# Kernel optimization log

Hardware: AMD Instinct MI355X
Metric: run time of the kernel (lower is better)

## Reference

```python
import jax, jax.numpy as jnp
import numpy as np

DIM = 256
NUM_HEADS = 8
NUM_NEI = (16, 32)
G = len(NUM_NEI)          # branches
G_H = NUM_HEADS // G      # heads per branch = 4
G_DIM = DIM // G          # channels per branch = 128
HD = G_DIM // G_H         # head dim = 32
SCALE = HD ** (-0.5)
M_MSF = G                 # MSF branches
CHANNEL = DIM // M_MSF    # 128
D_MSF = CHANNEL           # r=1

gelu = lambda t: jax.nn.gelu(t, approximate=False)


def setup_inputs() -> dict:
    key = jax.random.key(0)
    ks = jax.random.split(key, 16)
    B, N = 4, 2048
    s = lambda fan: fan ** (-0.5)
    inp = {
        "x": jax.random.normal(ks[0], (B, N, DIM), jnp.float32),
        "pos": jax.random.uniform(ks[1], (B, N, 3), jnp.float32),
        # qkv linear (no bias); stored as (in, out)
        "Wqkv": jax.random.normal(ks[2], (DIM, 3 * DIM), jnp.float32) * s(DIM),
        # per-branch rel-pos MLPs: Linear(3, g_dim) + GELU
        "Wp0": jax.random.normal(ks[3], (3, G_DIM), jnp.float32) * s(3),
        "bp0": jnp.zeros((G_DIM,), jnp.float32),
        "Wp1": jax.random.normal(ks[4], (3, G_DIM), jnp.float32) * s(3),
        "bp1": jnp.zeros((G_DIM,), jnp.float32),
        # MSF params
        "W_proj": jax.random.normal(ks[5], (DIM, DIM), jnp.float32) * s(DIM),
        "b_proj": jnp.zeros((DIM,), jnp.float32),
        "W_fc1": jax.random.normal(ks[6], (DIM, D_MSF), jnp.float32) * s(DIM),
        "b_fc1": jnp.zeros((D_MSF,), jnp.float32),
        "W_fc2": jax.random.normal(ks[7], (D_MSF, M_MSF * CHANNEL), jnp.float32) * s(D_MSF),
        "b_fc2": jnp.zeros((M_MSF * CHANNEL,), jnp.float32),
        "W_head": jax.random.normal(ks[8], (DIM, DIM), jnp.float32) * s(DIM),
        "b_head": jnp.zeros((DIM,), jnp.float32),
    }
    return inp


def _branch(q, k, v, pos, knn_idx, Wp, bp):
    """One head-group: KNN gather + rel-pos MLP fused attention.
    q,k,v: [B,N,g_dim]; pos: [B,N,3]; knn_idx: [B,N,nk]."""
    B, N, g_dim = k.shape
    nk = knn_idx.shape[-1]
    gather = jax.vmap(lambda t, idx: t[idx])  # per-batch fancy gather -> [B,N,nk,D]
    knn_xyz = gather(pos, knn_idx)                       # [B,N,nk,3]
    kg = gather(k, knn_idx)                              # [B,N,nk,g_dim]
    vg = gather(v, knn_idx)
    # split heads: b n k (h d) -> b h n k d
    split = lambda t: t.reshape(B, N, nk, G_H, HD).transpose(0, 3, 1, 2, 4)
    kg, vg = split(kg), split(vg)
    rel = pos[:, :, None, :] - knn_xyz                   # [B,N,nk,3]
    vrp = split(gelu(rel @ Wp + bp))                     # [B,h,N,nk,d]
    vg = vg + vrp
    attn_rel = vrp.sum(-1)                               # [B,h,N,nk]
    qh = q.reshape(B, N, G_H, HD).transpose(0, 2, 1, 3)  # [B,h,N,d]
    logits = jnp.einsum('bhnd,bhnkd->bhnk', qh, kg) * SCALE + attn_rel
    a = jax.nn.softmax(logits, axis=-1)
    out = jnp.einsum('bhnk,bhnkd->bhnd', a, vg)          # [B,h,N,d]
    return out.transpose(0, 2, 1, 3).reshape(B, N, g_dim)


def _msf(x, W_proj, b_proj, W_fc1, b_fc1, W_fc2, b_fc2, W_head, b_head):
    bs, N, dim = x.shape
    input_groups = x.transpose(0, 2, 1).reshape(bs, M_MSF, CHANNEL, N)
    feats_proj = gelu(x @ W_proj + b_proj)               # [bs,N,dim]
    feats_S = feats_proj.mean(axis=1)                    # global avg pool over N -> [bs,dim]
    feats_Z = gelu(feats_S @ W_fc1 + b_fc1)
    av = (feats_Z @ W_fc2 + b_fc2).reshape(bs, M_MSF, CHANNEL, 1)
    av = jax.nn.softmax(av, axis=1)                      # softmax over branches
    feats_V = (input_groups * av).reshape(bs, dim, N).transpose(0, 2, 1)
    feats_V = feats_V @ W_head + b_head
    return feats_proj + feats_V


def reference(x, pos, Wqkv, Wp0, bp0, Wp1, bp1,
              W_proj, b_proj, W_fc1, b_fc1, W_fc2, b_fc2, W_head, b_head):
    B, N, C = x.shape
    # pairwise squared distances [B,N,N] (broadcast form, as in source)
    dists = jnp.sum((pos[:, :, None, :] - pos[:, None, :, :]) ** 2, axis=-1)
    order = jnp.argsort(dists, axis=-1)                  # [B,N,N]
    qkv = (x @ Wqkv).reshape(B, N, 3, C).transpose(2, 0, 1, 3)  # [3,B,N,C]
    pos_params = [(Wp0, bp0), (Wp1, bp1)]
    outs = []
    for i, nk in enumerate(NUM_NEI):
        sl = slice(i * G_DIM, (i + 1) * G_DIM)
        q, k, v = qkv[0][..., sl], qkv[1][..., sl], qkv[2][..., sl]
        knn_idx = order[:, :, :nk]
        Wp, bp = pos_params[i]
        outs.append(_branch(q, k, v, pos, knn_idx, Wp, bp))
    xcat = jnp.concatenate(outs, axis=-1)                # [B,N,C]
    return _msf(xcat, W_proj, b_proj, W_fc1, b_fc1, W_fc2, b_fc2, W_head, b_head)
```

## Files before the change

### kernel.cpp

```cpp
#include <hip/hip_runtime.h>
#include <cstdint>
#include <cstddef>

#define B_    4
#define NPT   2048
#define DIM_  256
#define QKVW  768
#define XLEN  2097152
#define QLEN  196608
#define PLEN  65536
#define TOTC  (XLEN + QLEN + 2 * PLEN)

typedef unsigned short ushort_t;
typedef unsigned long long u64;
typedef short bf16x8 __attribute__((ext_vector_type(8)));
typedef float f32x4 __attribute__((ext_vector_type(4)));

__device__ __forceinline__ float gelu_f(float x) {
  return 0.5f * x * (1.0f + erff(x * 0.70710678118654752440f));
}

__device__ __forceinline__ float gelu_fast(float x) {
  const float is2 = 0.70710678118654752440f;
  float z = x * is2;
  float az = __builtin_fabsf(z);
  float t = __builtin_amdgcn_rcpf(fmaf(0.3275911f, az, 1.0f));
  float p = fmaf(1.061405429f, t, -1.453152027f);
  p = fmaf(p, t, 1.421413741f);
  p = fmaf(p, t, -0.284496736f);
  p = fmaf(p, t, 0.254829592f);
  p = p * t;
  float e = __expf(-az * az);
  float er = fmaf(-p, e, 1.0f);
  er = __builtin_copysignf(er, x);
  return 0.5f * x * (1.0f + er);
}

__device__ __forceinline__ ushort_t f2bf(float f) {
  unsigned u = __float_as_uint(f);
  unsigned r = (u + 0x7fffu + ((u >> 16) & 1u)) >> 16;
  return (ushort_t)r;
}
__device__ __forceinline__ float bf2f(ushort_t h) {
  return __uint_as_float(((unsigned)h) << 16);
}
__device__ __forceinline__ float bflo(unsigned p) {
  return __uint_as_float(p << 16);
}
__device__ __forceinline__ float bfhi(unsigned p) {
  return __uint_as_float(p & 0xffff0000u);
}

__device__ __forceinline__ float bfly16_sum(float x) {
  x += __int_as_float(__builtin_amdgcn_ds_swizzle(__float_as_int(x), 0x041F));
  x += __int_as_float(__builtin_amdgcn_ds_swizzle(__float_as_int(x), 0x081F));
  x += __int_as_float(__builtin_amdgcn_ds_swizzle(__float_as_int(x), 0x101F));
  x += __int_as_float(__builtin_amdgcn_ds_swizzle(__float_as_int(x), 0x201F));
  return x;
}

__device__ __forceinline__ bf16x8 scale_bf(bf16x8 v, const float* avk) {
  bf16x8 r;
#pragma unroll
  for (int e = 0; e < 8; e++) {
    float f = bf2f((ushort_t)v[e]) * avk[e];
    r[e] = (short)f2bf(f);
  }
  return r;
}

__global__ __launch_bounds__(256) void convert_kernel(
    const float* __restrict__ x, const float* __restrict__ Wqkv,
    const float* __restrict__ Wproj, const float* __restrict__ Whead,
    ushort_t* __restrict__ xbf, ushort_t* __restrict__ WqkvT,
    ushort_t* __restrict__ WprojT, ushort_t* __restrict__ WheadT,
    float* __restrict__ part) {
  int base = blockIdx.x * 256 + threadIdx.x;
  if (base < 1024) part[base] = 0.f;
  for (int i = base; i < TOTC; i += 2048 * 256) {
    if (i < XLEN) {
      xbf[i] = f2bf(x[i]);
    } else if (i < XLEN + QLEN) {
      int e = i - XLEN;
      int k = e / 768, n = e - k * 768;
      WqkvT[n * 256 + k] = f2bf(Wqkv[e]);
    } else if (i < XLEN + QLEN + PLEN) {
      int e = i - XLEN - QLEN;
      int k = e >> 8, n = e & 255;
      WprojT[n * 256 + k] = f2bf(Wproj[e]);
    } else {
      int e = i - XLEN - QLEN - PLEN;
      int k = e >> 8, n = e & 255;
      WheadT[n * 256 + k] = f2bf(Whead[e]);
    }
  }
}

__global__ __launch_bounds__(256) void knn_gemm0_kernel(
    const float* __restrict__ pos, int* __restrict__ idx_out,
    const ushort_t* __restrict__ A, const ushort_t* __restrict__ BT,
    ushort_t* __restrict__ C) {
  __shared__ u64 buf[3][128];
  int tid = threadIdx.x;
  int w = tid >> 6, lane = tid & 63;
  if (w == 3) {
    constexpr int K = 256;
    constexpr int N = 768;
    int quad = lane >> 4, r16 = lane & 15;
    int t0 = blockIdx.x;
    int m0 = (t0 / 24) * 64, n0 = (t0 % 24) * 32;
    const ushort_t* Ap = A + (size_t)(m0 + r16) * K + quad * 8;
    const ushort_t* Bp = BT + (size_t)(n0 + r16) * K + quad * 8;
    f32x4 acc[4][2] = {};
    bf16x8 af[4], bfv[2], af2[4], bf2[2];
#pragma unroll
    for (int i = 0; i < 4; i++) af[i] = *(const bf16x8*)(Ap + (size_t)i * 16 * K);
#pragma unroll
    for (int j = 0; j < 2; j++) bfv[j] = *(const bf16x8*)(Bp + (size_t)j * 16 * K);
#pragma unroll
    for (int kc = 0; kc < 8; kc++) {
      if (kc < 7) {
        int ko = (kc + 1) * 32;
#pragma unroll
        for (int i = 0; i < 4; i++)
          af2[i] = *(const bf16x8*)(Ap + (size_t)i * 16 * K + ko);
#pragma unroll
        for (int j = 0; j < 2; j++)
          bf2[j] = *(const bf16x8*)(Bp + (size_t)j * 16 * K + ko);
      }
#pragma unroll
      for (int i = 0; i < 4; i++) {
        acc[i][0] = __builtin_amdgcn_mfma_f32_16x16x32_bf16(af[i], bfv[0], acc[i][0], 0, 0, 0);
        acc[i][1] = __builtin_amdgcn_mfma_f32_16x16x32_bf16(af[i], bfv[1], acc[i][1], 0, 0, 0);
      }
#pragma unroll
      for (int i = 0; i < 4; i++) af[i] = af2[i];
      bfv[0] = bf2[0]; bfv[1] = bf2[1];
    }
#pragma unroll
    for (int i = 0; i < 4; i++) {
#pragma unroll
      for (int j = 0; j < 2; j++) {
        int col = n0 + j * 16 + r16;
#pragma unroll
        for (int r = 0; r < 4; r++) {
          int row = m0 + i * 16 + quad * 4 + r;
          C[(size_t)row * N + col] = f2bf(acc[i][j][r]);
        }
      }
    }
    return;
  }
  int wq = blockIdx.x * 3 + w;
  if (wq >= 8192) return;
  int b = wq >> 11, n = wq & (NPT - 1);
  const float* pb = pos + (size_t)b * NPT * 3;
  float qx = pb[n * 3 + 0], qy = pb[n * 3 + 1], qz = pb[n * 3 + 2];
  float dist[32];
  {
#pragma clang fp contract(off)
#pragma unroll
    for (int s = 0; s < 32; s++) {
      int j = lane + (s << 6);
      float dx = qx - pb[j * 3 + 0];
      float dy = qy - pb[j * 3 + 1];
      float dz = qz - pb[j * 3 + 2];
      float d = dx * dx;
      d = d + dy * dy;
      d = d + dz * dz;
      dist[s] = d;
    }
  }
  unsigned lo = 0x3C000000u;
  unsigned hi = 0x3E800001u;
  for (int it = 0; it < 31 && hi - lo > 1; ++it) {
    unsigned mid = (lo + hi) >> 1;
    float fm = __uint_as_float(mid);
    int c = 0;
#pragma unroll
    for (int s = 0; s < 32; s++)
      c += (int)__popcll(__ballot(dist[s] < fm));
    if (c >= 32) { hi = mid; if (c <= 64) break; }
    else lo = mid;
  }
  float fT = __uint_as_float(hi);
  buf[w][lane] = ~0ULL;
  buf[w][lane + 64] = ~0ULL;
  __builtin_amdgcn_wave_barrier();
  asm volatile("s_waitcnt lgkmcnt(0)" ::: "memory");
  unsigned base = 0;
#pragma unroll
  for (int s = 0; s < 32; s++) {
    bool m = dist[s] < fT;
    u64 bal = __ballot(m);
    unsigned pre = __builtin_amdgcn_mbcnt_hi(
        (unsigned)(bal >> 32), __builtin_amdgcn_mbcnt_lo((unsigned)bal, 0u));
    unsigned p = base + pre;
    if (m && p < 128u) {
      int j = lane + (s << 6);
      buf[w][p] = ((u64)__float_as_uint(dist[s]) << 32) | (unsigned)j;
    }
    base += (unsigned)__popcll(bal);
  }
  __builtin_amdgcn_wave_barrier();
  asm volatile("s_waitcnt lgkmcnt(0)" ::: "memory");
  unsigned total = base;
  if (total > 128u) total = 128u;
  unsigned mt = (total + 7u) & ~7u;
  u64 k0 = buf[w][lane];
  u64 k1 = buf[w][lane + 64];
  int r0 = 0, r1 = 0;
  for (unsigned i = 0; i < mt; i += 8) {
#pragma unroll
    for (int t = 0; t < 8; t++) {
      u64 ki = buf[w][i + t];
      r0 += (ki < k0) ? 1 : 0;
      r1 += (ki < k1) ? 1 : 0;
    }
  }
  if (r0 < 32) idx_out[(size_t)wq * 32 + r0] = (int)(unsigned)(k0 & 0xffffffffULL);
  if (r1 < 32) idx_out[(size_t)wq * 32 + r1] = (int)(unsigned)(k1 & 0xffffffffULL);
}

template <int MODE>
__global__ __launch_bounds__(64, 4) void gemm_rf(
    const ushort_t* __restrict__ A, const ushort_t* __restrict__ BT,
    const float* __restrict__ bias, const float* __restrict__ extra,
    float* __restrict__ C, float* __restrict__ part,
    const float* __restrict__ av, int N) {
  constexpr int K = 256;
  int lane = threadIdx.x;
  int quad = lane >> 4, r16 = lane & 15;
  int t0 = blockIdx.x;
  int m0 = (t0 >> 3) * 64, n0 = (t0 & 7) * 32;
  int batch = m0 >> 11;
  const ushort_t* Ap = A + (size_t)(m0 + r16) * K + quad * 8;
  const ushort_t* Bp = BT + (size_t)(n0 + r16) * K + quad * 8;
  f32x4 acc[4][2] = {};
  bf16x8 af[4], bf[2], af2[4], bf2[2];
#pragma unroll
  for (int i = 0; i < 4; i++) af[i] = *(const bf16x8*)(Ap + (size_t)i * 16 * K);
#pragma unroll
  for (int j = 0; j < 2; j++) bf[j] = *(const bf16x8*)(Bp + (size_t)j * 16 * K);
#pragma unroll
  for (int kc = 0; kc < 8; kc++) {
    if (kc < 7) {
      int ko = (kc + 1) * 32;
#pragma unroll
      for (int i = 0; i < 4; i++)
        af2[i] = *(const bf16x8*)(Ap + (size_t)i * 16 * K + ko);
#pragma unroll
      for (int j = 0; j < 2; j++)
        bf2[j] = *(const bf16x8*)(Bp + (size_t)j * 16 * K + ko);
    }
    bf16x8 b0 = bf[0], b1 = bf[1];
    if (MODE == 2) {
      const float* avk = av + batch * 256 + kc * 32 + quad * 8;
      b0 = scale_bf(b0, avk);
      b1 = scale_bf(b1, avk);
    }
#pragma unroll
    for (int i = 0; i < 4; i++) {
      acc[i][0] = __builtin_amdgcn_mfma_f32_16x16x32_bf16(af[i], b0, acc[i][0], 0, 0, 0);
      acc[i][1] = __builtin_amdgcn_mfma_f32_16x16x32_bf16(af[i], b1, acc[i][1], 0, 0, 0);
    }
#pragma unroll
    for (int i = 0; i < 4; i++) af[i] = af2[i];
    bf[0] = bf2[0]; bf[1] = bf2[1];
  }
  float cs[2] = {};
#pragma unroll
  for (int i = 0; i < 4; i++) {
#pragma unroll
    for (int j = 0; j < 2; j++) {
      int col = n0 + j * 16 + r16;
#pragma unroll
      for (int r = 0; r < 4; r++) {
        int row = m0 + i * 16 + quad * 4 + r;
        float v = acc[i][j][r];
        if (MODE == 1) { v = gelu_fast(v + bias[col]); cs[j] += v; }
        else if (MODE == 2) v = extra[(size_t)row * 256 + col] + v + bias[col];
        C[(size_t)row * N + col] = v;
      }
    }
  }
  if (MODE == 1) {
#pragma unroll
    for (int j = 0; j < 2; j++) {
      cs[j] += __shfl_xor(cs[j], 16, 64);
      cs[j] += __shfl_xor(cs[j], 32, 64);
    }
    if (quad == 0) {
#pragma unroll
      for (int j = 0; j < 2; j++)
        atomicAdd(&part[batch * 256 + n0 + j * 16 + r16], cs[j]);
    }
  }
}

template <int NK>
__device__ __forceinline__ void attn_core(
    const ushort_t* __restrict__ kvbase, int lane, const int* sidx,
    const float4* srel, float qSx, float qSy,
    float2 w0, float2 w1, float2 w2, float2 bb,
    float& num0, float& num1, float& den) {
#pragma unroll
  for (int j = 0; j < NK; j++) {
    int jj = __builtin_amdgcn_readfirstlane(sidx[j]);
    float4 rr = srel[j];
    const ushort_t* kb = kvbase + (size_t)jj * QKVW;
    unsigned pk = ((const unsigned*)kb)[lane];
    unsigned pv = ((const unsigned*)(kb + 256))[lane];
    float kvx = bflo(pk), kvy = bfhi(pk);
    float vvx = bflo(pv), vvy = bfhi(pv);
    float x0 = fmaf(rr.x, w0.x, fmaf(rr.y, w1.x, fmaf(rr.z, w2.x, bb.x)));
    float x1 = fmaf(rr.x, w0.y, fmaf(rr.y, w1.y, fmaf(rr.z, w2.y, bb.y)));
    float z0 = x0 * fmaf(0.0713548163f, x0 * x0, 1.5957691216f);
    float z1 = x1 * fmaf(0.0713548163f, x1 * x1, 1.5957691216f);
    float r0 = x0 * __builtin_amdgcn_rcpf(1.0f + __expf(-z0));
    float r1 = x1 * __builtin_amdgcn_rcpf(1.0f + __expf(-z1));
    float p = fmaf(qSx, kvx, r0) + fmaf(qSy, kvy, r1);
    float logit = bfly16_sum(p);
    float e = __expf(logit);
    den += e;
    num0 = fmaf(e, vvx + r0, num0);
    num1 = fmaf(e, vvy + r1, num1);
  }
}

__global__ __launch_bounds__(64) void attn_kernel(
    const ushort_t* __restrict__ qkv, const float* __restrict__ pos,
    const int* __restrict__ knn,
    const float* __restrict__ Wp0, const float* __restrict__ bp0,
    const float* __restrict__ Wp1, const float* __restrict__ bp1,
    ushort_t* __restrict__ xcat) {
  const float SCALE = 0.17677669529663687f;
  int u = blockIdx.x;
  int g = blockIdx.y;
  int b = u >> 11, n = u & (NPT - 1);
  int lane = threadIdx.x;
  int c2 = lane * 2;
  __shared__ int s_idx[32];
  __shared__ float4 s_rel[32];
  const ushort_t* qkvb = qkv + (size_t)b * NPT * QKVW;
  if (lane < 32) {
    int j = knn[(size_t)u * 32 + lane];
    s_idx[lane] = j;
    const float* pn = pos + ((size_t)b * NPT + n) * 3;
    const float* pj = pos + ((size_t)b * NPT + j) * 3;
    s_rel[lane] = make_float4(pn[0] - pj[0], pn[1] - pj[1],
                              pn[2] - pj[2], 0.f);
  }
  __builtin_amdgcn_wave_barrier();
  asm volatile("s_waitcnt lgkmcnt(0)" ::: "memory");
  const float* Wp = g ? Wp1 : Wp0;
  const float* bp = g ? bp1 : bp0;
  float2 w0 = *(const float2*)(Wp + c2);
  float2 w1 = *(const float2*)(Wp + 128 + c2);
  float2 w2 = *(const float2*)(Wp + 256 + c2);
  float2 bb = *(const float2*)(bp + c2);
  unsigned pq = ((const unsigned*)(qkvb + (size_t)n * QKVW + g * 128))[lane];
  float qSx = bflo(pq) * SCALE, qSy = bfhi(pq) * SCALE;
  const ushort_t* kvbase = qkvb + 256 + g * 128;
  float num0 = 0.f, num1 = 0.f, den = 0.f;
  if (g == 0)
    attn_core<16>(kvbase, lane, s_idx, s_rel, qSx, qSy, w0, w1, w2, bb,
                  num0, num1, den);
  else
    attn_core<32>(kvbase, lane, s_idx, s_rel, qSx, qSy, w0, w1, w2, bb,
                  num0, num1, den);
  float inv = __builtin_amdgcn_rcpf(den);
  unsigned pk = (unsigned)f2bf(num0 * inv) | ((unsigned)f2bf(num1 * inv) << 16);
  ((unsigned*)xcat)[((size_t)b * NPT + n) * 128 + g * 64 + lane] = pk;
}

__global__ __launch_bounds__(256) void msf_av_kernel(
    const float* __restrict__ part, const float* __restrict__ Wfc1,
    const float* __restrict__ bfc1, const float* __restrict__ Wfc2,
    const float* __restrict__ bfc2, float* __restrict__ av_out) {
  int b = blockIdx.x, t = threadIdx.x;
  __shared__ float S[256], Z[128], A[256];
  S[t] = part[b * 256 + t] * (1.0f / 2048.0f);
  __syncthreads();
  if (t < 128) {
    float z = bfc1[t];
    for (int i = 0; i < 256; i++) z += S[i] * Wfc1[i * 128 + t];
    Z[t] = gelu_f(z);
  }
  __syncthreads();
  float a = bfc2[t];
  for (int j = 0; j < 128; j++) a += Z[j] * Wfc2[j * 256 + t];
  A[t] = a;
  __syncthreads();
  float pA = A[t ^ 128];
  float m = fmaxf(a, pA);
  float e = expf(a - m);
  av_out[b * 256 + t] = e / (e + expf(pA - m));
}

extern "C" void kernel_launch(void* const* d_in, const int* in_sizes, int n_in,
                              void* d_out, int out_size, void* d_ws, size_t ws_size,
                              hipStream_t stream) {
  const float* x     = (const float*)d_in[0];
  const float* pos   = (const float*)d_in[1];
  const float* Wqkv  = (const float*)d_in[2];
  const float* Wp0   = (const float*)d_in[3];
  const float* bp0   = (const float*)d_in[4];
  const float* Wp1   = (const float*)d_in[5];
  const float* bp1   = (const float*)d_in[6];
  const float* Wproj = (const float*)d_in[7];
  const float* bproj = (const float*)d_in[8];
  const float* Wfc1  = (const float*)d_in[9];
  const float* bfc1  = (const float*)d_in[10];
  const float* Wfc2  = (const float*)d_in[11];
  const float* bfc2  = (const float*)d_in[12];
  const float* Whead = (const float*)d_in[13];
  const float* bhead = (const float*)d_in[14];
  float* out = (float*)d_out;

  char* ws = (char*)d_ws;
  size_t off = 0;
  int* idx = (int*)(ws + off);              off += (size_t)B_ * NPT * 32 * 4;
  ushort_t* qkv = (ushort_t*)(ws + off);
  float* fp = (float*)(ws + off);
  off += (size_t)B_ * NPT * QKVW * 4;
  ushort_t* xbf = (ushort_t*)(ws + off);    off += (size_t)B_ * NPT * DIM_ * 2;
  ushort_t* xcat = xbf;
  ushort_t* WqkvT = (ushort_t*)(ws + off);  off += (size_t)QLEN * 2;
  ushort_t* WprojT = (ushort_t*)(ws + off); off += (size_t)PLEN * 2;
  ushort_t* WheadT = (ushort_t*)(ws + off); off += (size_t)PLEN * 2;
  float* part = (float*)(ws + off);         off += 1024 * 4;
  float* av = (float*)(ws + off);           off += 1024 * 4;

  const int M = B_ * NPT;

  convert_kernel<<<2048, 256, 0, stream>>>(x, Wqkv, Wproj, Whead,
                                           xbf, WqkvT, WprojT, WheadT, part);
  knn_gemm0_kernel<<<3072, 256, 0, stream>>>(pos, idx, xbf, WqkvT, qkv);
  attn_kernel<<<dim3(M, 2), 64, 0, stream>>>(qkv, pos, idx,
                                             Wp0, bp0, Wp1, bp1, xcat);
  gemm_rf<1><<<1024, 64, 0, stream>>>(xcat, WprojT, bproj, nullptr,
                                      fp, part, nullptr, DIM_);
  msf_av_kernel<<<B_, 256, 0, stream>>>(part, Wfc1, bfc1, Wfc2, bfc2, av);
  gemm_rf<2><<<1024, 64, 0, stream>>>(xcat, WheadT, bhead, fp,
                                      out, nullptr, av, DIM_);
}
```

Measured before the change: 185.2 us.

## Process two KNN queries per wave and remap attention blocks for XCD locality

The fused KNN+QKV-GEMM kernel now uses two waves per block for KNN, each handling two query points that share the position loads, and two waves for GEMM tiles. The grid drops from 3072 to 2048 blocks. The attention kernel's block index is remapped so that each XCD's blocks touch a single batch, which should improve L2 locality for the gathered K/V. The cost is higher register pressure from the doubled distance arrays, and the bisections now run one after the other inside each wave.

```diff
diff --git a/kernel.cpp b/kernel.cpp
--- a/kernel.cpp
+++ b/kernel.cpp
@@ -57,6 +57,11 @@
   x += __int_as_float(__builtin_amdgcn_ds_swizzle(__float_as_int(x), 0x101F));
   x += __int_as_float(__builtin_amdgcn_ds_swizzle(__float_as_int(x), 0x201F));
   return x;
+}
+
+__device__ __forceinline__ unsigned mbcnt64(u64 bal) {
+  return __builtin_amdgcn_mbcnt_hi(
+      (unsigned)(bal >> 32), __builtin_amdgcn_mbcnt_lo((unsigned)bal, 0u));
 }
 
 __device__ __forceinline__ bf16x8 scale_bf(bf16x8 v, const float* avk) {
@@ -100,14 +105,15 @@
     const float* __restrict__ pos, int* __restrict__ idx_out,
     const ushort_t* __restrict__ A, const ushort_t* __restrict__ BT,
     ushort_t* __restrict__ C) {
-  __shared__ u64 buf[3][128];
+  __shared__ u64 buf[4][128];
   int tid = threadIdx.x;
   int w = tid >> 6, lane = tid & 63;
-  if (w == 3) {
+  if (w >= 2) {
+    int t0 = blockIdx.x * 2 + (w - 2);
+    if (t0 >= 3072) return;
     constexpr int K = 256;
     constexpr int N = 768;
     int quad = lane >> 4, r16 = lane & 15;
-    int t0 = blockIdx.x;
     int m0 = (t0 / 24) * 64, n0 = (t0 % 24) * 32;
     const ushort_t* Ap = A + (size_t)(m0 + r16) * K + quad * 8;
     const ushort_t* Bp = BT + (size_t)(n0 + r16) * K + quad * 8;
@@ -151,75 +157,92 @@
     }
     return;
   }
-  int wq = blockIdx.x * 3 + w;
-  if (wq >= 8192) return;
-  int b = wq >> 11, n = wq & (NPT - 1);
+  int wqA = blockIdx.x * 4 + w * 2;
+  int wqB = wqA + 1;
+  int b = wqA >> 11;
+  int nA = wqA & (NPT - 1), nB = wqB & (NPT - 1);
   const float* pb = pos + (size_t)b * NPT * 3;
-  float qx = pb[n * 3 + 0], qy = pb[n * 3 + 1], qz = pb[n * 3 + 2];
-  float dist[32];
+  float qx0 = pb[nA * 3 + 0], qy0 = pb[nA * 3 + 1], qz0 = pb[nA * 3 + 2];
+  float qx1 = pb[nB * 3 + 0], qy1 = pb[nB * 3 + 1], qz1 = pb[nB * 3 + 2];
+  float d0[32], d1[32];
   {
 #pragma clang fp contract(off)
 #pragma unroll
     for (int s = 0; s < 32; s++) {
       int j = lane + (s << 6);
-      float dx = qx - pb[j * 3 + 0];
-      float dy = qy - pb[j * 3 + 1];
-      float dz = qz - pb[j * 3 + 2];
-      float d = dx * dx;
-      d = d + dy * dy;
-      d = d + dz * dz;
-      dist[s] = d;
-    }
-  }
-  unsigned lo = 0x3C000000u;
-  unsigned hi = 0x3E800001u;
-  for (int it = 0; it < 31 && hi - lo > 1; ++it) {
-    unsigned mid = (lo + hi) >> 1;
-    float fm = __uint_as_float(mid);
-    int c = 0;
-#pragma unroll
-    for (int s = 0; s < 32; s++)
-      c += (int)__popcll(__ballot(dist[s] < fm));
-    if (c >= 32) { hi = mid; if (c <= 64) break; }
-    else lo = mid;
-  }
-  float fT = __uint_as_float(hi);
-  buf[w][lane] = ~0ULL;
-  buf[w][lane + 64] = ~0ULL;
+      float px = pb[j * 3 + 0], py = pb[j * 3 + 1], pz = pb[j * 3 + 2];
+      float ax = qx0 - px, ay = qy0 - py, az = qz0 - pz;
+      float bx = qx1 - px, by = qy1 - py, bz = qz1 - pz;
+      float da = ax * ax;
+      da = da + ay * ay;
+      da = da + az * az;
+      float db = bx * bx;
+      db = db + by * by;
+      db = db + bz * bz;
+      d0[s] = da;
+      d1[s] = db;
+    }
+  }
+  auto bisect = [&](const float (&dd)[32]) -> float {
+    unsigned lo = 0x3C000000u;
+    unsigned hi = 0x3E800001u;
+    for (int it = 0; it < 31 && hi - lo > 1; ++it) {
+      unsigned mid = (lo + hi) >> 1;
+      float fm = __uint_as_float(mid);
+      int c = 0;
+#pragma unroll
+      for (int s = 0; s < 32; s++)
+        c += (int)__popcll(__ballot(dd[s] < fm));
+      if (c >= 32) { hi = mid; if (c <= 64) break; }
+      else lo = mid;
+    }
+    return __uint_as_float(hi);
+  };
+  float fT0 = bisect(d0);
+  float fT1 = bisect(d1);
+  int s0 = w * 2, s1 = w * 2 + 1;
+  buf[s0][lane] = ~0ULL; buf[s0][lane + 64] = ~0ULL;
+  buf[s1][lane] = ~0ULL; buf[s1][lane + 64] = ~0ULL;
   __builtin_amdgcn_wave_barrier();
   asm volatile("s_waitcnt lgkmcnt(0)" ::: "memory");
-  unsigned base = 0;
+  unsigned c0 = 0, c1 = 0;
 #pragma unroll
   for (int s = 0; s < 32; s++) {
-    bool m = dist[s] < fT;
-    u64 bal = __ballot(m);
-    unsigned pre = __builtin_amdgcn_mbcnt_hi(
-        (unsigned)(bal >> 32), __builtin_amdgcn_mbcnt_lo((unsigned)bal, 0u));
-    unsigned p = base + pre;
-    if (m && p < 128u) {
-      int j = lane + (s << 6);
-      buf[w][p] = ((u64)__float_as_uint(dist[s]) << 32) | (unsigned)j;
-    }
-    base += (unsigned)__popcll(bal);
+    int j = lane + (s << 6);
+    bool m0 = d0[s] < fT0, m1 = d1[s] < fT1;
+    u64 bal0 = __ballot(m0), bal1 = __ballot(m1);
+    unsigned p0 = c0 + mbcnt64(bal0), p1 = c1 + mbcnt64(bal1);
+    if (m0 && p0 < 128u)
+      buf[s0][p0] = ((u64)__float_as_uint(d0[s]) << 32) | (unsigned)j;
+    if (m1 && p1 < 128u)
+      buf[s1][p1] = ((u64)__float_as_uint(d1[s]) << 32) | (unsigned)j;
+    c0 += (unsigned)__popcll(bal0);
+    c1 += (unsigned)__popcll(bal1);
   }
   __builtin_amdgcn_wave_barrier();
   asm volatile("s_waitcnt lgkmcnt(0)" ::: "memory");
-  unsigned total = base;
-  if (total > 128u) total = 128u;
-  unsigned mt = (total + 7u) & ~7u;
-  u64 k0 = buf[w][lane];
-  u64 k1 = buf[w][lane + 64];
-  int r0 = 0, r1 = 0;
+  if (c0 > 128u) c0 = 128u;
+  if (c1 > 128u) c1 = 128u;
+  unsigned mt0 = (c0 + 7u) & ~7u, mt1 = (c1 + 7u) & ~7u;
+  unsigned mt = mt0 > mt1 ? mt0 : mt1;
+  u64 k0A = buf[s0][lane], k1A = buf[s0][lane + 64];
+  u64 k0B = buf[s1][lane], k1B = buf[s1][lane + 64];
+  int r0A = 0, r1A = 0, r0B = 0, r1B = 0;
   for (unsigned i = 0; i < mt; i += 8) {
 #pragma unroll
     for (int t = 0; t < 8; t++) {
-      u64 ki = buf[w][i + t];
-      r0 += (ki < k0) ? 1 : 0;
-      r1 += (ki < k1) ? 1 : 0;
-    }
-  }
-  if (r0 < 32) idx_out[(size_t)wq * 32 + r0] = (int)(unsigned)(k0 & 0xffffffffULL);
-  if (r1 < 32) idx_out[(size_t)wq * 32 + r1] = (int)(unsigned)(k1 & 0xffffffffULL);
+      u64 kiA = buf[s0][i + t];
+      u64 kiB = buf[s1][i + t];
+      r0A += (kiA < k0A) ? 1 : 0;
+      r1A += (kiA < k1A) ? 1 : 0;
+      r0B += (kiB < k0B) ? 1 : 0;
+      r1B += (kiB < k1B) ? 1 : 0;
+    }
+  }
+  if (r0A < 32) idx_out[(size_t)wqA * 32 + r0A] = (int)(unsigned)(k0A & 0xffffffffULL);
+  if (r1A < 32) idx_out[(size_t)wqA * 32 + r1A] = (int)(unsigned)(k1A & 0xffffffffULL);
+  if (r0B < 32) idx_out[(size_t)wqB * 32 + r0B] = (int)(unsigned)(k0B & 0xffffffffULL);
+  if (r1B < 32) idx_out[(size_t)wqB * 32 + r1B] = (int)(unsigned)(k1B & 0xffffffffULL);
 }
 
 template <int MODE>
@@ -335,9 +358,12 @@
     const float* __restrict__ Wp1, const float* __restrict__ bp1,
     ushort_t* __restrict__ xcat) {
   const float SCALE = 0.17677669529663687f;
-  int u = blockIdx.x;
+  int bid = blockIdx.x;
+  int xcd = bid & 7;
+  int b = xcd >> 1;
+  int n = ((bid >> 3) << 1) | (xcd & 1);
+  int u = (b << 11) | n;
   int g = blockIdx.y;
-  int b = u >> 11, n = u & (NPT - 1);
   int lane = threadIdx.x;
   int c2 = lane * 2;
   __shared__ int s_idx[32];
@@ -436,7 +462,7 @@
 
   convert_kernel<<<2048, 256, 0, stream>>>(x, Wqkv, Wproj, Whead,
                                            xbf, WqkvT, WprojT, WheadT, part);
-  knn_gemm0_kernel<<<3072, 256, 0, stream>>>(pos, idx, xbf, WqkvT, qkv);
+  knn_gemm0_kernel<<<2048, 256, 0, stream>>>(pos, idx, xbf, WqkvT, qkv);
   attn_kernel<<<dim3(M, 2), 64, 0, stream>>>(qkv, pos, idx,
                                              Wp0, bp0, Wp1, bp1, xcat);
   gemm_rf<1><<<1024, 64, 0, stream>>>(xcat, WprojT, bproj, nullptr,
```

After: 209.6 us. +13.2%, slower.
